# Kernel optimization log

Hardware: AMD Instinct MI355X
Metric: run time of the kernel (lower is better)

Reference implementation:

```python
import jax, jax.numpy as jnp
import numpy as np

B, C, H, W = 4, 256, 64, 64
G = 8
EPS = 1e-5


def setup_inputs() -> dict:
    key = jax.random.key(0)
    ks = jax.random.split(key, 6)
    s = 0.02  # small init so softmax isn't saturated
    return {
        "x": jax.random.normal(ks[0], (B, C, H, W), dtype=jnp.float32),
        "gn_scale": jnp.ones((C,), jnp.float32),
        "gn_bias": jnp.zeros((C,), jnp.float32),
        "Wq": jax.random.normal(ks[1], (C, C), jnp.float32) * s,
        "bq": jnp.zeros((C,), jnp.float32),
        "Wk": jax.random.normal(ks[2], (C, C), jnp.float32) * s,
        "bk": jnp.zeros((C,), jnp.float32),
        "Wv": jax.random.normal(ks[3], (C, C), jnp.float32) * s,
        "bv": jnp.zeros((C,), jnp.float32),
        "Wf": jax.random.normal(ks[4], (C, C), jnp.float32) * s,
        "bf": jnp.zeros((C,), jnp.float32),
    }


def group_norm(x, scale, bias):
    # x: [B, C, H, W] -> normalize over (C/G, H, W) per group
    b, c, h, w = x.shape
    xg = x.reshape(b, G, c // G, h, w)
    mu = xg.mean(axis=(2, 3, 4), keepdims=True)
    var = xg.var(axis=(2, 3, 4), keepdims=True)
    xg = (xg - mu) * jax.lax.rsqrt(var + EPS)
    xn = xg.reshape(b, c, h, w)
    return xn * scale[None, :, None, None] + bias[None, :, None, None]


def reference(x, gn_scale, gn_bias, Wq, bq, Wk, bk, Wv, bv, Wf, bf):
    b, c, h, w = x.shape
    residual = x
    xn = group_norm(x, gn_scale, gn_bias)
    xf = xn.reshape(b, c, h * w)                      # [B, C, N]
    # 1x1 conv1d == channel matmul
    Q = jnp.einsum('oc,bcn->bon', Wq, xf) + bq[None, :, None]
    K = jnp.einsum('oc,bcn->bon', Wk, xf) + bk[None, :, None]
    V = jnp.einsum('oc,bcn->bon', Wv, xf) + bv[None, :, None]
    scale = c ** (-0.5)
    # scores[b, i, j] = Q[b,:,i] . K[b,:,j]
    scores = jnp.einsum('bci,bcj->bij', Q, K) * scale  # [B, N, N]
    attn = jax.nn.softmax(scores, axis=-1)
    # Output = bmm(V, attn^T): out[b,c,i] = sum_j V[b,c,j] * attn[b,i,j]
    out = jnp.einsum('bcj,bij->bci', V, attn)          # [B, C, N]
    out = jnp.einsum('oc,bcn->bon', Wf, out) + bf[None, :, None]
    return out.reshape(b, c, h, w) + residual
```

## Files before the change

### kernel.cpp

```cpp
#include <hip/hip_runtime.h>
#include <hip/hip_bf16.h>

#define BATCH 4
#define CCH   256
#define NPOS  4096
#define NGRP  8
#define CPG   32
#define KVB   32
#define QB    256
#define NSPLIT 4
#define JLEN  (NPOS / NSPLIT)
#define NITER (JLEN / KVB)

typedef __attribute__((ext_vector_type(8))) short bfx8;
typedef __attribute__((ext_vector_type(4))) float f32x4;
typedef __attribute__((ext_vector_type(2))) unsigned int u32x2;
typedef __attribute__((ext_vector_type(4))) unsigned int u32x4;

__device__ __forceinline__ short f2bf(float f){
    unsigned u = __builtin_bit_cast(unsigned, f);
    u += 0x7fffu + ((u >> 16) & 1u);
    return (short)(u >> 16);
}
__device__ __forceinline__ float bf2f(short s){
    unsigned u = ((unsigned)(unsigned short)s) << 16;
    return __builtin_bit_cast(float, u);
}

__global__ __launch_bounds__(256) void gn_stats(
    const float* __restrict__ x, float* __restrict__ psum)
{
    const int bg = blockIdx.x, p = blockIdx.y;
    const size_t base = (size_t)bg * (CPG * NPOS) + (size_t)p * 16384;
    const float4* x4 = (const float4*)(x + base);
    float s = 0.f, s2 = 0.f;
    for (int i = threadIdx.x; i < 4096; i += 256) {
        float4 v = x4[i];
        s  += v.x + v.y + v.z + v.w;
        s2 += v.x*v.x + v.y*v.y + v.z*v.z + v.w*v.w;
    }
    for (int off = 32; off; off >>= 1) {
        s  += __shfl_down(s,  off);
        s2 += __shfl_down(s2, off);
    }
    __shared__ float rs[4], rs2[4];
    const int t = threadIdx.x;
    if ((t & 63) == 0) { rs[t >> 6] = s; rs2[t >> 6] = s2; }
    __syncthreads();
    if (t == 0) {
        psum[(bg*8 + p)*2 + 0] = rs[0] + rs[1] + rs[2] + rs[3];
        psum[(bg*8 + p)*2 + 1] = rs2[0] + rs2[1] + rs2[2] + rs2[3];
    }
}

__global__ __launch_bounds__(256) void gn_apply(
    const float* __restrict__ x, const float* __restrict__ gamma,
    const float* __restrict__ beta, const float* __restrict__ psum,
    short* __restrict__ xnb)
{
    const int ch = blockIdx.x, bg = blockIdx.y;
    const int b = bg >> 3, g = bg & 7;
    float S = 0.f, S2 = 0.f;
    #pragma unroll
    for (int p = 0; p < 8; p++) {
        S  += psum[(bg*8 + p)*2 + 0];
        S2 += psum[(bg*8 + p)*2 + 1];
    }
    const float inv = 1.0f / (float)(CPG * NPOS);
    const float mu = S * inv;
    const float rstd = rsqrtf(S2 * inv - mu * mu + 1e-5f);

    __shared__ float T[32][132];
    const int t = threadIdx.x;
    const int c = t >> 3;
    const int gc = g * CPG + c;
    const float ga = gamma[gc] * rstd;
    const float be = beta[gc] - mu * ga;
    const float* xr = &x[((size_t)b * CCH + gc) * NPOS + ch * 128];
    #pragma unroll
    for (int k = 0; k < 4; k++) {
        const int nl = (t & 7) * 16 + k * 4;
        float4 v = *(const float4*)&xr[nl];
        v.x = v.x * ga + be; v.y = v.y * ga + be;
        v.z = v.z * ga + be; v.w = v.w * ga + be;
        *(float4*)&T[c][nl] = v;
    }
    __syncthreads();
    const int n = t >> 1, hf = t & 1;
    short* orow = &xnb[((size_t)b * NPOS + ch * 128 + n) * CCH + g * CPG + hf * 16];
    bfx8 o0, o1;
    #pragma unroll
    for (int e = 0; e < 8; e++) {
        o0[e] = f2bf(T[hf*16 + e][n]);
        o1[e] = f2bf(T[hf*16 + 8 + e][n]);
    }
    *(bfx8*)&orow[0] = o0;
    *(bfx8*)&orow[8] = o1;
}

template<int MODE>
__global__ __launch_bounds__(256, 2) void gemm_mfma(
    const float* __restrict__ W, const short* __restrict__ Xb,
    const float* __restrict__ bias, const float* __restrict__ resid,
    short* __restrict__ Yb, float* __restrict__ Yf, float scale)
{
    __shared__ short Wl[128 * 32];
    __shared__ short Xl[128 * 32];
    const int t = threadIdx.x, l = t & 63, w = t >> 6;
    const int lg = l >> 4, ln = l & 15;
    const int b = blockIdx.z;
    const int n0 = blockIdx.x * 128, o0 = blockIdx.y * 128;
    const int wo = (w & 1) * 64, wn = (w >> 1) * 64;
    const short* Xg = Xb + ((size_t)b * NPOS + n0) * CCH;

    f32x4 acc[4][4];
    #pragma unroll
    for (int i = 0; i < 4; i++)
        #pragma unroll
        for (int j = 0; j < 4; j++) acc[i][j] = (f32x4){0.f,0.f,0.f,0.f};

    const int srow = t >> 2;
    const int cb   = (t & 3) * 8;

    for (int kk = 0; kk < CCH; kk += 32) {
        bfx8 xst[2], wst[2];
        #pragma unroll
        for (int k = 0; k < 2; k++) {
            const int row = srow + k * 64;
            xst[k] = *(const bfx8*)&Xg[(size_t)row * CCH + kk + cb];
            const float4 wa = *(const float4*)&W[(size_t)(o0 + row) * CCH + kk + cb];
            const float4 wb = *(const float4*)&W[(size_t)(o0 + row) * CCH + kk + cb + 4];
            wst[k] = (bfx8){ f2bf(wa.x), f2bf(wa.y), f2bf(wa.z), f2bf(wa.w),
                             f2bf(wb.x), f2bf(wb.y), f2bf(wb.z), f2bf(wb.w) };
        }
        __syncthreads();
        #pragma unroll
        for (int k = 0; k < 2; k++) {
            const int row = srow + k * 64;
            *(bfx8*)&Xl[row * 32 + cb] = xst[k];
            *(bfx8*)&Wl[row * 32 + cb] = wst[k];
        }
        __syncthreads();

        bfx8 xf[4], wf[4];
        #pragma unroll
        for (int i = 0; i < 4; i++) {
            xf[i] = *(const bfx8*)&Xl[(wn + i*16 + ln) * 32 + lg * 8];
            wf[i] = *(const bfx8*)&Wl[(wo + i*16 + ln) * 32 + lg * 8];
        }
        #pragma unroll
        for (int i = 0; i < 4; i++)
            #pragma unroll
            for (int j = 0; j < 4; j++) {
                if constexpr (MODE == 0)
                    acc[i][j] = __builtin_amdgcn_mfma_f32_16x16x32_bf16(xf[i], wf[j], acc[i][j], 0,0,0);
                else
                    acc[i][j] = __builtin_amdgcn_mfma_f32_16x16x32_bf16(wf[i], xf[j], acc[i][j], 0,0,0);
            }
    }

    if constexpr (MODE == 0) {
        float bv[4];
        #pragma unroll
        for (int j = 0; j < 4; j++) bv[j] = bias[o0 + wo + j*16 + ln];
        #pragma unroll
        for (int i = 0; i < 4; i++)
            #pragma unroll
            for (int r = 0; r < 4; r++) {
                const int n = n0 + wn + i*16 + lg*4 + r;
                short* dst = &Yb[((size_t)b * NPOS + n) * CCH + o0 + wo];
                #pragma unroll
                for (int j = 0; j < 4; j++)
                    dst[j*16 + ln] = f2bf((acc[i][j][r] + bv[j]) * scale);
            }
    } else {
        #pragma unroll
        for (int i = 0; i < 4; i++)
            #pragma unroll
            for (int r = 0; r < 4; r++) {
                const int o = o0 + wo + i*16 + lg*4 + r;
                const float bv = bias[o];
                const size_t base = ((size_t)b * CCH + o) * NPOS + n0 + wn;
                #pragma unroll
                for (int j = 0; j < 4; j++) {
                    if constexpr (MODE == 1)
                        Yb[base + j*16 + ln] = f2bf(acc[i][j][r] + bv);
                    else
                        Yf[base + j*16 + ln] = acc[i][j][r] + bv + resid[base + j*16 + ln];
                }
            }
    }
}

#define SOFTMAX_MT(SA, SB, mreg, lreg, accA, paOut) do { \
    float tm_ = fmaxf(fmaxf(fmaxf(SA[0],SA[1]),fmaxf(SA[2],SA[3])), \
                      fmaxf(fmaxf(SB[0],SB[1]),fmaxf(SB[2],SB[3]))); \
    tm_ = fmaxf(tm_, __shfl_xor(tm_, 16)); \
    tm_ = fmaxf(tm_, __shfl_xor(tm_, 32)); \
    if (__any(tm_ > mreg)) { \
        const float mn_ = fmaxf(mreg, tm_); \
        const float al_ = __expf(mreg - mn_); \
        mreg = mn_; lreg *= al_; \
        const f32x4 alv_ = { __shfl(al_, lg*4+0), __shfl(al_, lg*4+1), \
                             __shfl(al_, lg*4+2), __shfl(al_, lg*4+3) }; \
        _Pragma("unroll") \
        for (int dt_ = 0; dt_ < 16; dt_++) accA[dt_] *= alv_; \
    } \
    const float p0_ = __expf(SA[0]-mreg), p1_ = __expf(SA[1]-mreg); \
    const float p2_ = __expf(SA[2]-mreg), p3_ = __expf(SA[3]-mreg); \
    const float p4_ = __expf(SB[0]-mreg), p5_ = __expf(SB[1]-mreg); \
    const float p6_ = __expf(SB[2]-mreg), p7_ = __expf(SB[3]-mreg); \
    float ps_ = ((p0_+p1_)+(p2_+p3_)) + ((p4_+p5_)+(p6_+p7_)); \
    ps_ += __shfl_xor(ps_, 16); ps_ += __shfl_xor(ps_, 32); \
    lreg += ps_; \
    paOut = (bfx8){ f2bf(p0_), f2bf(p1_), f2bf(p2_), f2bf(p3_), \
                    f2bf(p4_), f2bf(p5_), f2bf(p6_), f2bf(p7_) }; \
} while (0)

__global__ __launch_bounds__(512, 2) void attn_mfma(
    const short* __restrict__ Qt, const short* __restrict__ Kt,
    const short* __restrict__ Vc, short* __restrict__ Op0,
    short* __restrict__ Op123, float* __restrict__ Mp, float* __restrict__ Lp)
{
    __shared__ short Ks[32 * 256];
    __shared__ short Vt[256 * 40];

    const int t = threadIdx.x;
    const int l = t & 63, w = t >> 6;
    const int lg = l >> 4, ln = l & 15;
    const int h = blockIdx.y, b = blockIdx.z;
    const size_t bo = (size_t)b * NPOS * CCH;
    const short* Qg = Qt + bo;
    const short* Kg = Kt + bo;
    const short* Vg = Vc + bo;
    short* Op = (h == 0) ? Op0 : (Op123 + (size_t)(h - 1) * BATCH * NPOS * CCH);

    const int qbase = blockIdx.x * QB + w * 32;

    bfx8 qf0[8], qf1[8];
    #pragma unroll
    for (int kt = 0; kt < 8; kt++) {
        qf0[kt] = *(const bfx8*)&Qg[(size_t)(qbase + ln) * CCH + kt*32 + lg*8];
        qf1[kt] = *(const bfx8*)&Qg[(size_t)(qbase + 16 + ln) * CCH + kt*32 + lg*8];
    }

    f32x4 acc0[16], acc1[16];
    #pragma unroll
    for (int dt = 0; dt < 16; dt++) {
        acc0[dt] = (f32x4){0.f,0.f,0.f,0.f};
        acc1[dt] = (f32x4){0.f,0.f,0.f,0.f};
    }
    float m0 = -1e30f, l0 = 0.f, m1 = -1e30f, l1 = 0.f;
    const int j0base = h * JLEN;

    for (int s = 0; s < NITER; s++) {
        const int j0 = j0base + s * KVB;
        bfx8 kst[2], vst[2];
        int jK[2], cK[2], dV[2], jV[2];
        #pragma unroll
        for (int k = 0; k < 2; k++) {
            const int idx = t + k * 512;
            jK[k] = idx >> 5;          cK[k] = (idx & 31) * 8;
            dV[k] = idx >> 2;          jV[k] = (idx & 3) * 8;
            kst[k] = *(const bfx8*)&Kg[(size_t)(j0 + jK[k]) * CCH + cK[k]];
            vst[k] = *(const bfx8*)&Vg[(size_t)dV[k] * NPOS + j0 + jV[k]];
        }
        __syncthreads();
        #pragma unroll
        for (int k = 0; k < 2; k++) {
            *(bfx8*)&Ks[jK[k] * 256 + (cK[k] ^ ((jK[k] & 7) << 3))] = kst[k];
            *(bfx8*)&Vt[dV[k] * 40 + jV[k]] = vst[k];
        }
        __syncthreads();

        f32x4 S00 = (f32x4){0,0,0,0}, S01 = (f32x4){0,0,0,0};
        f32x4 S10 = (f32x4){0,0,0,0}, S11 = (f32x4){0,0,0,0};
        #pragma unroll
        for (int kt = 0; kt < 8; kt++) {
            const int cA = (kt*32 + lg*8) ^ ((ln & 7) << 3);
            const bfx8 kf0 = *(const bfx8*)&Ks[ln * 256 + cA];
            const bfx8 kf1 = *(const bfx8*)&Ks[(16 + ln) * 256 + cA];
            S00 = __builtin_amdgcn_mfma_f32_16x16x32_bf16(kf0, qf0[kt], S00, 0,0,0);
            S01 = __builtin_amdgcn_mfma_f32_16x16x32_bf16(kf1, qf0[kt], S01, 0,0,0);
            S10 = __builtin_amdgcn_mfma_f32_16x16x32_bf16(kf0, qf1[kt], S10, 0,0,0);
            S11 = __builtin_amdgcn_mfma_f32_16x16x32_bf16(kf1, qf1[kt], S11, 0,0,0);
        }

        bfx8 pa0, pa1;
        SOFTMAX_MT(S00, S01, m0, l0, acc0, pa0);
        SOFTMAX_MT(S10, S11, m1, l1, acc1, pa1);

        #pragma unroll
        for (int dt = 0; dt < 16; dt++) {
            const int d = dt*16 + ln;
            const u32x2 v0 = *(const u32x2*)&Vt[d * 40 + lg*4];
            const u32x2 v1 = *(const u32x2*)&Vt[d * 40 + 16 + lg*4];
            const bfx8 vf = __builtin_bit_cast(bfx8, (u32x4){ v0[0], v0[1], v1[0], v1[1] });
            acc0[dt] = __builtin_amdgcn_mfma_f32_16x16x32_bf16(pa0, vf, acc0[dt], 0,0,0);
            acc1[dt] = __builtin_amdgcn_mfma_f32_16x16x32_bf16(pa1, vf, acc1[dt], 0,0,0);
        }
    }

    {
        const float inv0 = 1.0f / l0;
        const f32x4 lv = { __shfl(inv0, lg*4+0), __shfl(inv0, lg*4+1),
                           __shfl(inv0, lg*4+2), __shfl(inv0, lg*4+3) };
        #pragma unroll
        for (int dt = 0; dt < 16; dt++) {
            const f32x4 o = acc0[dt] * lv;
            const int d = dt*16 + ln;
            #pragma unroll
            for (int r = 0; r < 4; r++)
                Op[((size_t)b * NPOS + qbase + lg*4 + r) * CCH + d] = f2bf(o[r]);
        }
        if (lg == 0) {
            Mp[((size_t)h * BATCH + b) * NPOS + qbase + ln] = m0;
            Lp[((size_t)h * BATCH + b) * NPOS + qbase + ln] = l0;
        }
    }
    {
        const float inv1 = 1.0f / l1;
        const f32x4 lv = { __shfl(inv1, lg*4+0), __shfl(inv1, lg*4+1),
                           __shfl(inv1, lg*4+2), __shfl(inv1, lg*4+3) };
        #pragma unroll
        for (int dt = 0; dt < 16; dt++) {
            const f32x4 o = acc1[dt] * lv;
            const int d = dt*16 + ln;
            #pragma unroll
            for (int r = 0; r < 4; r++)
                Op[((size_t)b * NPOS + qbase + 16 + lg*4 + r) * CCH + d] = f2bf(o[r]);
        }
        if (lg == 0) {
            Mp[((size_t)h * BATCH + b) * NPOS + qbase + 16 + ln] = m1;
            Lp[((size_t)h * BATCH + b) * NPOS + qbase + 16 + ln] = l1;
        }
    }
}

__global__ __launch_bounds__(256) void combine4(
    const short* __restrict__ Op0, const short* __restrict__ Op123,
    const float* __restrict__ Mp, const float* __restrict__ Lp,
    short* __restrict__ AO)
{
    const int b  = blockIdx.y;
    const int q0 = blockIdx.x * 64;
    const int t  = threadIdx.x;
    __shared__ float wgt[4][64];
    if (t < 64) {
        const size_t qi = (size_t)b * NPOS + q0 + t;
        float mm[4], ll[4];
        #pragma unroll
        for (int hh = 0; hh < 4; hh++) {
            mm[hh] = Mp[(size_t)hh * BATCH * NPOS + qi];
            ll[hh] = Lp[(size_t)hh * BATCH * NPOS + qi];
        }
        const float M = fmaxf(fmaxf(mm[0], mm[1]), fmaxf(mm[2], mm[3]));
        float e[4], sum = 0.f;
        #pragma unroll
        for (int hh = 0; hh < 4; hh++) { e[hh] = __expf(mm[hh] - M) * ll[hh]; sum += e[hh]; }
        const float invs = 1.0f / sum;
        #pragma unroll
        for (int hh = 0; hh < 4; hh++) wgt[hh][t] = e[hh] * invs;
    }
    __syncthreads();
    const size_t hs = (size_t)BATCH * NPOS * CCH;
    #pragma unroll
    for (int i = 0; i < 8; i++) {
        const int flat = i * 256 + t;
        const int q = flat >> 5;
        const int cb = (flat & 31) * 8;
        const size_t row = ((size_t)b * NPOS + q0 + q) * CCH + cb;
        const float w0 = wgt[0][q], w1 = wgt[1][q], w2 = wgt[2][q], w3 = wgt[3][q];
        const bfx8 a0 = *(const bfx8*)&Op0[row];
        const bfx8 a1 = *(const bfx8*)&Op123[row];
        const bfx8 a2 = *(const bfx8*)&Op123[hs + row];
        const bfx8 a3 = *(const bfx8*)&Op123[2*hs + row];
        bfx8 ov;
        #pragma unroll
        for (int e = 0; e < 8; e++)
            ov[e] = f2bf(w0*bf2f(a0[e]) + w1*bf2f(a1[e]) + w2*bf2f(a2[e]) + w3*bf2f(a3[e]));
        *(bfx8*)&AO[row] = ov;
    }
}

extern "C" void kernel_launch(void* const* d_in, const int* in_sizes, int n_in,
                              void* d_out, int out_size, void* d_ws, size_t ws_size,
                              hipStream_t stream)
{
    const float* x   = (const float*)d_in[0];
    const float* gns = (const float*)d_in[1];
    const float* gnb = (const float*)d_in[2];
    const float* Wq  = (const float*)d_in[3];
    const float* bq  = (const float*)d_in[4];
    const float* Wk  = (const float*)d_in[5];
    const float* bk  = (const float*)d_in[6];
    const float* Wv  = (const float*)d_in[7];
    const float* bv  = (const float*)d_in[8];
    const float* Wf  = (const float*)d_in[9];
    const float* bf  = (const float*)d_in[10];
    float* out = (float*)d_out;
    char* wsb  = (char*)d_ws;

    short* xnb   = (short*)(wsb);
    short* Op0   = (short*)(wsb);
    short* Qt    = (short*)(wsb + (8  << 20));
    short* Kt    = (short*)(wsb + (16 << 20));
    short* Vc    = (short*)(wsb + (24 << 20));
    short* Op123 = (short*)(wsb + (32 << 20));
    float* Mp    = (float*)(wsb + (56 << 20));
    float* Lp    = Mp + (size_t)NSPLIT * BATCH * NPOS;
    float* psum  = Lp + (size_t)NSPLIT * BATCH * NPOS;
    short* AO    = Qt;

    gn_stats<<<dim3(BATCH * NGRP, 8), 256, 0, stream>>>(x, psum);
    gn_apply<<<dim3(NPOS / 128, BATCH * NGRP), 256, 0, stream>>>(x, gns, gnb, psum, xnb);

    dim3 gg(NPOS / 128, CCH / 128, BATCH);
    gemm_mfma<0><<<gg, 256, 0, stream>>>(Wq, xnb, bq, nullptr, Qt, nullptr, 0.0625f);
    gemm_mfma<0><<<gg, 256, 0, stream>>>(Wk, xnb, bk, nullptr, Kt, nullptr, 1.f);
    gemm_mfma<1><<<gg, 256, 0, stream>>>(Wv, xnb, bv, nullptr, Vc, nullptr, 1.f);

    attn_mfma<<<dim3(NPOS / QB, NSPLIT, BATCH), 512, 0, stream>>>(
        Qt, Kt, Vc, Op0, Op123, Mp, Lp);

    combine4<<<dim3(NPOS / 64, BATCH), 256, 0, stream>>>(Op0, Op123, Mp, Lp, AO);

    gemm_mfma<2><<<gg, 256, 0, stream>>>(Wf, AO, bf, x, nullptr, out, 1.f);
}
```

Baseline: 245.9 us.

## Double-buffer GEMM and attention loads, pre-convert weights, lazy softmax rescale

Weight matrices are converted to bf16 once in extra blocks of the stats kernel instead of inside every GEMM tile. The projection GEMMs move to 64x128 tiles with a K step of 64, swizzled double-buffered LDS and vectorized epilogues. Attention drops to 256-thread blocks over 128 queries, stages K asynchronously with global_load_lds into a double buffer, and prefetches V in registers. Softmax skips rescaling unless the running max grows by more than 4, and the MFMA operand order is swapped so each lane's output is one row, avoiding shuffles. The risks are lower per-block reuse, more barriers, and bf16 overflow headroom from the lazy max.

```diff
diff --git a/kernel.cpp b/kernel.cpp
--- a/kernel.cpp
+++ b/kernel.cpp
@@ -7,12 +7,13 @@
 #define NGRP  8
 #define CPG   32
 #define KVB   32
-#define QB    256
+#define QB    128
 #define NSPLIT 4
 #define JLEN  (NPOS / NSPLIT)
 #define NITER (JLEN / KVB)
 
 typedef __attribute__((ext_vector_type(8))) short bfx8;
+typedef __attribute__((ext_vector_type(4))) short bfx4;
 typedef __attribute__((ext_vector_type(4))) float f32x4;
 typedef __attribute__((ext_vector_type(2))) unsigned int u32x2;
 typedef __attribute__((ext_vector_type(4))) unsigned int u32x4;
@@ -27,14 +28,44 @@
     return __builtin_bit_cast(float, u);
 }
 
+typedef const __attribute__((address_space(1))) unsigned int* as1_u32p;
+typedef __attribute__((address_space(3))) unsigned int* as3_u32p;
+
+__device__ __forceinline__ void async_cp16(short* lds, const short* g) {
+    __builtin_amdgcn_global_load_lds((as1_u32p)(unsigned long long)g,
+                                     (as3_u32p)(unsigned int)(unsigned long long)lds,
+                                     16, 0, 0);
+}
+
 __global__ __launch_bounds__(256) void gn_stats(
-    const float* __restrict__ x, float* __restrict__ psum)
+    const float* __restrict__ x, float* __restrict__ psum,
+    const float* __restrict__ Wq, const float* __restrict__ Wk,
+    const float* __restrict__ Wv, const float* __restrict__ Wf,
+    short* __restrict__ Wball)
 {
+    const int t = threadIdx.x;
+    if (blockIdx.y == 8) {
+        const int bx = blockIdx.x;
+        const int m = bx >> 3;
+        const float* src = (m == 0) ? Wq : (m == 1) ? Wk : (m == 2) ? Wv : Wf;
+        const int base = (bx & 7) * 8192;
+        short* dst = Wball + m * 65536;
+        #pragma unroll
+        for (int it = 0; it < 4; it++) {
+            const int idx = base + it * 2048 + t * 8;
+            const float4 a = *(const float4*)&src[idx];
+            const float4 b = *(const float4*)&src[idx + 4];
+            bfx8 o = { f2bf(a.x), f2bf(a.y), f2bf(a.z), f2bf(a.w),
+                       f2bf(b.x), f2bf(b.y), f2bf(b.z), f2bf(b.w) };
+            *(bfx8*)&dst[idx] = o;
+        }
+        return;
+    }
     const int bg = blockIdx.x, p = blockIdx.y;
     const size_t base = (size_t)bg * (CPG * NPOS) + (size_t)p * 16384;
     const float4* x4 = (const float4*)(x + base);
     float s = 0.f, s2 = 0.f;
-    for (int i = threadIdx.x; i < 4096; i += 256) {
+    for (int i = t; i < 4096; i += 256) {
         float4 v = x4[i];
         s  += v.x + v.y + v.z + v.w;
         s2 += v.x*v.x + v.y*v.y + v.z*v.z + v.w*v.w;
@@ -44,7 +75,6 @@
         s2 += __shfl_down(s2, off);
     }
     __shared__ float rs[4], rs2[4];
-    const int t = threadIdx.x;
     if ((t & 63) == 0) { rs[t >> 6] = s; rs2[t >> 6] = s2; }
     __syncthreads();
     if (t == 0) {
@@ -100,111 +130,141 @@
 
 template<int MODE>
 __global__ __launch_bounds__(256, 2) void gemm_mfma(
-    const float* __restrict__ W, const short* __restrict__ Xb,
+    const short* __restrict__ Wg, const short* __restrict__ Xb,
     const float* __restrict__ bias, const float* __restrict__ resid,
     short* __restrict__ Yb, float* __restrict__ Yf, float scale)
 {
-    __shared__ short Wl[128 * 32];
-    __shared__ short Xl[128 * 32];
+    __shared__ short Xl[2][64 * 64];
+    __shared__ short Wl[2][128 * 64];
     const int t = threadIdx.x, l = t & 63, w = t >> 6;
     const int lg = l >> 4, ln = l & 15;
     const int b = blockIdx.z;
-    const int n0 = blockIdx.x * 128, o0 = blockIdx.y * 128;
-    const int wo = (w & 1) * 64, wn = (w >> 1) * 64;
+    const int n0 = blockIdx.x * 64, o0 = blockIdx.y * 128;
+    const int wn = (w >> 1) * 32, wo = (w & 1) * 64;
     const short* Xg = Xb + ((size_t)b * NPOS + n0) * CCH;
 
-    f32x4 acc[4][4];
-    #pragma unroll
-    for (int i = 0; i < 4; i++)
+    f32x4 acc[2][4];
+    #pragma unroll
+    for (int i = 0; i < 2; i++)
         #pragma unroll
         for (int j = 0; j < 4; j++) acc[i][j] = (f32x4){0.f,0.f,0.f,0.f};
 
-    const int srow = t >> 2;
-    const int cb   = (t & 3) * 8;
-
-    for (int kk = 0; kk < CCH; kk += 32) {
-        bfx8 xst[2], wst[2];
-        #pragma unroll
-        for (int k = 0; k < 2; k++) {
-            const int row = srow + k * 64;
-            xst[k] = *(const bfx8*)&Xg[(size_t)row * CCH + kk + cb];
-            const float4 wa = *(const float4*)&W[(size_t)(o0 + row) * CCH + kk + cb];
-            const float4 wb = *(const float4*)&W[(size_t)(o0 + row) * CCH + kk + cb + 4];
-            wst[k] = (bfx8){ f2bf(wa.x), f2bf(wa.y), f2bf(wa.z), f2bf(wa.w),
-                             f2bf(wb.x), f2bf(wb.y), f2bf(wb.z), f2bf(wb.w) };
-        }
-        __syncthreads();
-        #pragma unroll
-        for (int k = 0; k < 2; k++) {
-            const int row = srow + k * 64;
-            *(bfx8*)&Xl[row * 32 + cb] = xst[k];
-            *(bfx8*)&Wl[row * 32 + cb] = wst[k];
-        }
-        __syncthreads();
-
-        bfx8 xf[4], wf[4];
+    bfx8 xs[2], ws4[4];
+    auto GLOAD = [&](int kk) {
+        #pragma unroll
+        for (int i = 0; i < 2; i++) {
+            const int L = i*256 + t;
+            xs[i] = *(const bfx8*)&Xg[(size_t)(L>>3)*CCH + kk + (L&7)*8];
+        }
         #pragma unroll
         for (int i = 0; i < 4; i++) {
-            xf[i] = *(const bfx8*)&Xl[(wn + i*16 + ln) * 32 + lg * 8];
-            wf[i] = *(const bfx8*)&Wl[(wo + i*16 + ln) * 32 + lg * 8];
-        }
-        #pragma unroll
-        for (int i = 0; i < 4; i++)
-            #pragma unroll
-            for (int j = 0; j < 4; j++) {
-                if constexpr (MODE == 0)
-                    acc[i][j] = __builtin_amdgcn_mfma_f32_16x16x32_bf16(xf[i], wf[j], acc[i][j], 0,0,0);
-                else
-                    acc[i][j] = __builtin_amdgcn_mfma_f32_16x16x32_bf16(wf[i], xf[j], acc[i][j], 0,0,0);
-            }
-    }
-
-    if constexpr (MODE == 0) {
-        float bv[4];
-        #pragma unroll
-        for (int j = 0; j < 4; j++) bv[j] = bias[o0 + wo + j*16 + ln];
-        #pragma unroll
-        for (int i = 0; i < 4; i++)
-            #pragma unroll
-            for (int r = 0; r < 4; r++) {
-                const int n = n0 + wn + i*16 + lg*4 + r;
-                short* dst = &Yb[((size_t)b * NPOS + n) * CCH + o0 + wo];
-                #pragma unroll
-                for (int j = 0; j < 4; j++)
-                    dst[j*16 + ln] = f2bf((acc[i][j][r] + bv[j]) * scale);
-            }
-    } else {
-        #pragma unroll
-        for (int i = 0; i < 4; i++)
-            #pragma unroll
-            for (int r = 0; r < 4; r++) {
-                const int o = o0 + wo + i*16 + lg*4 + r;
-                const float bv = bias[o];
-                const size_t base = ((size_t)b * CCH + o) * NPOS + n0 + wn;
+            const int L = i*256 + t;
+            ws4[i] = *(const bfx8*)&Wg[(size_t)(o0 + (L>>3))*CCH + kk + (L&7)*8];
+        }
+    };
+    auto WRITE = [&](int buf) {
+        #pragma unroll
+        for (int i = 0; i < 2; i++) {
+            const int L = i*256 + t; const int r = L>>3, c = (L&7)*8;
+            *(bfx8*)&Xl[buf][r*64 + (c ^ ((r&7)<<3))] = xs[i];
+        }
+        #pragma unroll
+        for (int i = 0; i < 4; i++) {
+            const int L = i*256 + t; const int r = L>>3, c = (L&7)*8;
+            *(bfx8*)&Wl[buf][r*64 + (c ^ ((r&7)<<3))] = ws4[i];
+        }
+    };
+
+    GLOAD(0); WRITE(0); __syncthreads();
+    int cur = 0;
+    const int swz = (ln & 7) << 3;
+    for (int step = 0; step < 4; step++) {
+        if (step < 3) GLOAD((step + 1) * 64);
+        #pragma unroll
+        for (int k2 = 0; k2 < 2; k2++) {
+            bfx8 xf[2], wf[4];
+            const int cb = (k2*32 + lg*8) ^ swz;
+            #pragma unroll
+            for (int i = 0; i < 2; i++)
+                xf[i] = *(const bfx8*)&Xl[cur][(wn + i*16 + ln)*64 + cb];
+            #pragma unroll
+            for (int j = 0; j < 4; j++)
+                wf[j] = *(const bfx8*)&Wl[cur][(wo + j*16 + ln)*64 + cb];
+            #pragma unroll
+            for (int i = 0; i < 2; i++)
                 #pragma unroll
                 for (int j = 0; j < 4; j++) {
-                    if constexpr (MODE == 1)
-                        Yb[base + j*16 + ln] = f2bf(acc[i][j][r] + bv);
+                    if constexpr (MODE == 0)
+                        acc[i][j] = __builtin_amdgcn_mfma_f32_16x16x32_bf16(wf[j], xf[i], acc[i][j], 0,0,0);
                     else
-                        Yf[base + j*16 + ln] = acc[i][j][r] + bv + resid[base + j*16 + ln];
+                        acc[i][j] = __builtin_amdgcn_mfma_f32_16x16x32_bf16(xf[i], wf[j], acc[i][j], 0,0,0);
+                }
+        }
+        if (step < 3) { WRITE(cur ^ 1); __syncthreads(); cur ^= 1; }
+    }
+
+    if constexpr (MODE == 0) {
+        #pragma unroll
+        for (int i = 0; i < 2; i++) {
+            const int n = n0 + wn + i*16 + ln;
+            short* dst = &Yb[((size_t)b * NPOS + n) * CCH + o0 + wo];
+            #pragma unroll
+            for (int j = 0; j < 4; j++) {
+                const float4 bv = *(const float4*)&bias[o0 + wo + j*16 + lg*4];
+                bfx4 pk = { f2bf((acc[i][j][0] + bv.x) * scale),
+                            f2bf((acc[i][j][1] + bv.y) * scale),
+                            f2bf((acc[i][j][2] + bv.z) * scale),
+                            f2bf((acc[i][j][3] + bv.w) * scale) };
+                *(bfx4*)&dst[j*16 + lg*4] = pk;
+            }
+        }
+    } else {
+        #pragma unroll
+        for (int j = 0; j < 4; j++) {
+            const int o = o0 + wo + j*16 + ln;
+            const float bv = bias[o];
+            #pragma unroll
+            for (int i = 0; i < 2; i++) {
+                const size_t base = ((size_t)b * CCH + o) * NPOS + n0 + wn + i*16 + lg*4;
+                if constexpr (MODE == 1) {
+                    bfx4 pk = { f2bf(acc[i][j][0] + bv), f2bf(acc[i][j][1] + bv),
+                                f2bf(acc[i][j][2] + bv), f2bf(acc[i][j][3] + bv) };
+                    *(bfx4*)&Yb[base] = pk;
+                } else {
+                    const f32x4 rv = *(const f32x4*)&resid[base];
+                    f32x4 v = acc[i][j];
+                    v[0] += bv + rv[0]; v[1] += bv + rv[1];
+                    v[2] += bv + rv[2]; v[3] += bv + rv[3];
+                    *(f32x4*)&Yf[base] = v;
                 }
             }
-    }
-}
+        }
+    }
+}
+
+#define STAGE_K(BUF, J0) do { \
+    short* kb_ = &Ks[BUF][0]; \
+    _Pragma("unroll") \
+    for (int i_ = 0; i_ < 4; i_++) { \
+        const int L_ = i_*256 + t; \
+        const int j_ = L_ >> 5; \
+        const int c_ = ((L_ & 31) << 3) ^ ((j_ & 7) << 3); \
+        async_cp16(&kb_[(i_*256 + (t & 192)) << 3], \
+                   &Kg[(size_t)((J0) + j_) * CCH + c_]); \
+    } \
+} while (0)
 
 #define SOFTMAX_MT(SA, SB, mreg, lreg, accA, paOut) do { \
     float tm_ = fmaxf(fmaxf(fmaxf(SA[0],SA[1]),fmaxf(SA[2],SA[3])), \
                       fmaxf(fmaxf(SB[0],SB[1]),fmaxf(SB[2],SB[3]))); \
     tm_ = fmaxf(tm_, __shfl_xor(tm_, 16)); \
     tm_ = fmaxf(tm_, __shfl_xor(tm_, 32)); \
-    if (__any(tm_ > mreg)) { \
+    if (__any(tm_ > mreg + 4.0f)) { \
         const float mn_ = fmaxf(mreg, tm_); \
         const float al_ = __expf(mreg - mn_); \
         mreg = mn_; lreg *= al_; \
-        const f32x4 alv_ = { __shfl(al_, lg*4+0), __shfl(al_, lg*4+1), \
-                             __shfl(al_, lg*4+2), __shfl(al_, lg*4+3) }; \
         _Pragma("unroll") \
-        for (int dt_ = 0; dt_ < 16; dt_++) accA[dt_] *= alv_; \
+        for (int dt_ = 0; dt_ < 16; dt_++) accA[dt_] *= al_; \
     } \
     const float p0_ = __expf(SA[0]-mreg), p1_ = __expf(SA[1]-mreg); \
     const float p2_ = __expf(SA[2]-mreg), p3_ = __expf(SA[3]-mreg); \
@@ -217,12 +277,12 @@
                     f2bf(p4_), f2bf(p5_), f2bf(p6_), f2bf(p7_) }; \
 } while (0)
 
-__global__ __launch_bounds__(512, 2) void attn_mfma(
+__global__ __launch_bounds__(256, 2) void attn_mfma(
     const short* __restrict__ Qt, const short* __restrict__ Kt,
     const short* __restrict__ Vc, short* __restrict__ Op0,
     short* __restrict__ Op123, float* __restrict__ Mp, float* __restrict__ Lp)
 {
-    __shared__ short Ks[32 * 256];
+    __shared__ short Ks[2][KVB * 256];
     __shared__ short Vt[256 * 40];
 
     const int t = threadIdx.x;
@@ -253,33 +313,43 @@
     float m0 = -1e30f, l0 = 0.f, m1 = -1e30f, l1 = 0.f;
     const int j0base = h * JLEN;
 
+    {
+        STAGE_K(0, j0base);
+        bfx8 vld[4];
+        #pragma unroll
+        for (int i = 0; i < 4; i++) {
+            const int L = i*256 + t;
+            vld[i] = *(const bfx8*)&Vg[(size_t)(L>>2) * NPOS + j0base + (L&3)*8];
+        }
+        #pragma unroll
+        for (int i = 0; i < 4; i++) {
+            const int L = i*256 + t;
+            *(bfx8*)&Vt[(L>>2) * 40 + (L&3)*8] = vld[i];
+        }
+        __syncthreads();
+    }
+
+    int cur = 0;
     for (int s = 0; s < NITER; s++) {
-        const int j0 = j0base + s * KVB;
-        bfx8 kst[2], vst[2];
-        int jK[2], cK[2], dV[2], jV[2];
-        #pragma unroll
-        for (int k = 0; k < 2; k++) {
-            const int idx = t + k * 512;
-            jK[k] = idx >> 5;          cK[k] = (idx & 31) * 8;
-            dV[k] = idx >> 2;          jV[k] = (idx & 3) * 8;
-            kst[k] = *(const bfx8*)&Kg[(size_t)(j0 + jK[k]) * CCH + cK[k]];
-            vst[k] = *(const bfx8*)&Vg[(size_t)dV[k] * NPOS + j0 + jV[k]];
-        }
-        __syncthreads();
-        #pragma unroll
-        for (int k = 0; k < 2; k++) {
-            *(bfx8*)&Ks[jK[k] * 256 + (cK[k] ^ ((jK[k] & 7) << 3))] = kst[k];
-            *(bfx8*)&Vt[dV[k] * 40 + jV[k]] = vst[k];
-        }
-        __syncthreads();
-
+        const int j0n = j0base + (s + 1) * KVB;
+        bfx8 vld[4];
+        if (s + 1 < NITER) {
+            STAGE_K(cur ^ 1, j0n);
+            #pragma unroll
+            for (int i = 0; i < 4; i++) {
+                const int L = i*256 + t;
+                vld[i] = *(const bfx8*)&Vg[(size_t)(L>>2) * NPOS + j0n + (L&3)*8];
+            }
+        }
+
+        const short* bK = &Ks[cur][0];
         f32x4 S00 = (f32x4){0,0,0,0}, S01 = (f32x4){0,0,0,0};
         f32x4 S10 = (f32x4){0,0,0,0}, S11 = (f32x4){0,0,0,0};
         #pragma unroll
         for (int kt = 0; kt < 8; kt++) {
             const int cA = (kt*32 + lg*8) ^ ((ln & 7) << 3);
-            const bfx8 kf0 = *(const bfx8*)&Ks[ln * 256 + cA];
-            const bfx8 kf1 = *(const bfx8*)&Ks[(16 + ln) * 256 + cA];
+            const bfx8 kf0 = *(const bfx8*)&bK[ln * 256 + cA];
+            const bfx8 kf1 = *(const bfx8*)&bK[(16 + ln) * 256 + cA];
             S00 = __builtin_amdgcn_mfma_f32_16x16x32_bf16(kf0, qf0[kt], S00, 0,0,0);
             S01 = __builtin_amdgcn_mfma_f32_16x16x32_bf16(kf1, qf0[kt], S01, 0,0,0);
             S10 = __builtin_amdgcn_mfma_f32_16x16x32_bf16(kf0, qf1[kt], S10, 0,0,0);
@@ -296,22 +366,30 @@
             const u32x2 v0 = *(const u32x2*)&Vt[d * 40 + lg*4];
             const u32x2 v1 = *(const u32x2*)&Vt[d * 40 + 16 + lg*4];
             const bfx8 vf = __builtin_bit_cast(bfx8, (u32x4){ v0[0], v0[1], v1[0], v1[1] });
-            acc0[dt] = __builtin_amdgcn_mfma_f32_16x16x32_bf16(pa0, vf, acc0[dt], 0,0,0);
-            acc1[dt] = __builtin_amdgcn_mfma_f32_16x16x32_bf16(pa1, vf, acc1[dt], 0,0,0);
-        }
+            acc0[dt] = __builtin_amdgcn_mfma_f32_16x16x32_bf16(vf, pa0, acc0[dt], 0,0,0);
+            acc1[dt] = __builtin_amdgcn_mfma_f32_16x16x32_bf16(vf, pa1, acc1[dt], 0,0,0);
+        }
+
+        __syncthreads();
+        if (s + 1 < NITER) {
+            #pragma unroll
+            for (int i = 0; i < 4; i++) {
+                const int L = i*256 + t;
+                *(bfx8*)&Vt[(L>>2) * 40 + (L&3)*8] = vld[i];
+            }
+        }
+        __syncthreads();
+        cur ^= 1;
     }
 
     {
         const float inv0 = 1.0f / l0;
-        const f32x4 lv = { __shfl(inv0, lg*4+0), __shfl(inv0, lg*4+1),
-                           __shfl(inv0, lg*4+2), __shfl(inv0, lg*4+3) };
+        short* orow = &Op[((size_t)b * NPOS + qbase + ln) * CCH];
         #pragma unroll
         for (int dt = 0; dt < 16; dt++) {
-            const f32x4 o = acc0[dt] * lv;
-            const int d = dt*16 + ln;
-            #pragma unroll
-            for (int r = 0; r < 4; r++)
-                Op[((size_t)b * NPOS + qbase + lg*4 + r) * CCH + d] = f2bf(o[r]);
+            const f32x4 o = acc0[dt] * inv0;
+            bfx4 pk = { f2bf(o[0]), f2bf(o[1]), f2bf(o[2]), f2bf(o[3]) };
+            *(bfx4*)&orow[dt*16 + lg*4] = pk;
         }
         if (lg == 0) {
             Mp[((size_t)h * BATCH + b) * NPOS + qbase + ln] = m0;
@@ -320,15 +398,12 @@
     }
     {
         const float inv1 = 1.0f / l1;
-        const f32x4 lv = { __shfl(inv1, lg*4+0), __shfl(inv1, lg*4+1),
-                           __shfl(inv1, lg*4+2), __shfl(inv1, lg*4+3) };
+        short* orow = &Op[((size_t)b * NPOS + qbase + 16 + ln) * CCH];
         #pragma unroll
         for (int dt = 0; dt < 16; dt++) {
-            const f32x4 o = acc1[dt] * lv;
-            const int d = dt*16 + ln;
-            #pragma unroll
-            for (int r = 0; r < 4; r++)
-                Op[((size_t)b * NPOS + qbase + 16 + lg*4 + r) * CCH + d] = f2bf(o[r]);
+            const f32x4 o = acc1[dt] * inv1;
+            bfx4 pk = { f2bf(o[0]), f2bf(o[1]), f2bf(o[2]), f2bf(o[3]) };
+            *(bfx4*)&orow[dt*16 + lg*4] = pk;
         }
         if (lg == 0) {
             Mp[((size_t)h * BATCH + b) * NPOS + qbase + 16 + ln] = m1;
@@ -403,27 +478,33 @@
 
     short* xnb   = (short*)(wsb);
     short* Op0   = (short*)(wsb);
-    short* Qt    = (short*)(wsb + (8  << 20));
-    short* Kt    = (short*)(wsb + (16 << 20));
-    short* Vc    = (short*)(wsb + (24 << 20));
-    short* Op123 = (short*)(wsb + (32 << 20));
-    float* Mp    = (float*)(wsb + (56 << 20));
+    short* Qt    = (short*)(wsb + (8u  << 20));
+    short* Kt    = (short*)(wsb + (16u << 20));
+    short* Vc    = (short*)(wsb + (24u << 20));
+    short* Op123 = (short*)(wsb + (32u << 20));
+    short* Wball = (short*)(wsb + (56u << 20));
+    float* Mp    = (float*)(wsb + (56u << 20) + (512u << 10));
     float* Lp    = Mp + (size_t)NSPLIT * BATCH * NPOS;
     float* psum  = Lp + (size_t)NSPLIT * BATCH * NPOS;
     short* AO    = Qt;
 
-    gn_stats<<<dim3(BATCH * NGRP, 8), 256, 0, stream>>>(x, psum);
+    const short* Wqb = Wball;
+    const short* Wkb = Wball + 65536;
+    const short* Wvb = Wball + 131072;
+    const short* Wfb = Wball + 196608;
+
+    gn_stats<<<dim3(BATCH * NGRP, 9), 256, 0, stream>>>(x, psum, Wq, Wk, Wv, Wf, Wball);
     gn_apply<<<dim3(NPOS / 128, BATCH * NGRP), 256, 0, stream>>>(x, gns, gnb, psum, xnb);
 
-    dim3 gg(NPOS / 128, CCH / 128, BATCH);
-    gemm_mfma<0><<<gg, 256, 0, stream>>>(Wq, xnb, bq, nullptr, Qt, nullptr, 0.0625f);
-    gemm_mfma<0><<<gg, 256, 0, stream>>>(Wk, xnb, bk, nullptr, Kt, nullptr, 1.f);
-    gemm_mfma<1><<<gg, 256, 0, stream>>>(Wv, xnb, bv, nullptr, Vc, nullptr, 1.f);
-
-    attn_mfma<<<dim3(NPOS / QB, NSPLIT, BATCH), 512, 0, stream>>>(
+    dim3 gg(NPOS / 64, CCH / 128, BATCH);
+    gemm_mfma<0><<<gg, 256, 0, stream>>>(Wqb, xnb, bq, nullptr, Qt, nullptr, 0.0625f);
+    gemm_mfma<0><<<gg, 256, 0, stream>>>(Wkb, xnb, bk, nullptr, Kt, nullptr, 1.f);
+    gemm_mfma<1><<<gg, 256, 0, stream>>>(Wvb, xnb, bv, nullptr, Vc, nullptr, 1.f);
+
+    attn_mfma<<<dim3(NPOS / QB, NSPLIT, BATCH), 256, 0, stream>>>(
         Qt, Kt, Vc, Op0, Op123, Mp, Lp);
 
     combine4<<<dim3(NPOS / 64, BATCH), 256, 0, stream>>>(Op0, Op123, Mp, Lp, AO);
 
-    gemm_mfma<2><<<gg, 256, 0, stream>>>(Wf, AO, bf, x, nullptr, out, 1.f);
-}
+    gemm_mfma<2><<<gg, 256, 0, stream>>>(Wfb, AO, bf, x, nullptr, out, 1.f);
+}
```

Measured after the change: 327.2 us. 33.0% more time.
